# Kernel optimization log

Hardware: AMD Instinct MI355X
Metric: run time of the kernel (lower is better)

Reference implementation:

```python
import jax, jax.numpy as jnp
import numpy as np

EPS = 1e-06

def _hermite_coeffs(coord_diff, sigmas):
    # coord_diff: [B,N,K,2], sigmas: [K] -> coeff: [B,N,K,6]
    dx = coord_diff[..., 0]  # [B,N,K]
    dy = coord_diff[..., 1]
    s2 = sigmas ** 2 + EPS   # [K], broadcasts over B,N
    s4 = sigmas ** 4 + EPS
    ones = jnp.ones_like(dx)
    # idx order follows nested (order, alpha) loop of the torch code:
    # (0,0), (0,1)->-dy, (1,0)->-dx, (0,2), (1,1), (2,0)
    coeff = jnp.stack([
        ones,
        -dy / s2,
        -dx / s2,
        dy ** 2 / s4 - 1.0 / s2,
        dx * dy / s4,
        dx ** 2 / s4 - 1.0 / s2,
    ], axis=-1)  # [B,N,K,6]
    return coeff


def setup_inputs() -> dict:
    key = jax.random.key(0)
    k1, k2, k3, k4, k5 = jax.random.split(key, 5)
    B, N, K, H, O = 4, 65536, 32, 6, 31
    return {
        "mlp_output": jax.random.normal(k1, (B, N, O), dtype=jnp.float32),
        "coord_diff": jax.random.normal(k2, (B, N, K, 2), dtype=jnp.float32),
        "sigmas": jax.random.uniform(k3, (K,), dtype=jnp.float32, minval=0.1, maxval=1.0),
        "gaussian_weights": jax.random.uniform(k4, (B, N, K), dtype=jnp.float32),
        "rbf_weights": jax.random.normal(k5, (K, H, O), dtype=jnp.float32),
    }


def reference(mlp_output, coord_diff, sigmas, gaussian_weights, rbf_weights):
    # final[b,n,o] = mlp_output[b,n,o] * sum_{k,h} coeff[b,n,k,h]*gw[b,n,k]*W[k,h,o]
    coeff = _hermite_coeffs(coord_diff, sigmas)            # [B,N,K,6]
    mix = jnp.einsum('bnkh,bnk,kho->bno', coeff, gaussian_weights, rbf_weights)
    return mlp_output * mix
```

## Files before the change

### kernel.cpp

```cpp
#include <hip/hip_runtime.h>

#define KK 32
#define HH 6
#define OO 31
#define KT 16
#define EPS 1e-6f

__global__ __launch_bounds__(256, 4) void hermite_fused_kernel(
    const float* __restrict__ mlp,
    const float* __restrict__ cd,
    const float* __restrict__ sigmas,
    const float* __restrict__ gw,
    const float* __restrict__ W,
    float* __restrict__ out,
    int P)
{
    __shared__ float s_i2[KK];
    __shared__ float s_i4[KK];

    const int tid = threadIdx.x;
    if (tid < KK) {
        float s = sigmas[tid];
        s_i2[tid] = 1.0f / (s * s + EPS);
        s_i4[tid] = 1.0f / (s * s * s * s + EPS);
    }
    __syncthreads();

    const int p = blockIdx.x * blockDim.x + tid;
    if (p >= P) return;

    const float4* __restrict__ cdv = (const float4*)(cd + (size_t)p * (KK * 2));
    const float4* __restrict__ gwv = (const float4*)(gw + (size_t)p * KK);

    float acc[OO];
#pragma unroll
    for (int o = 0; o < OO; ++o) acc[o] = 0.0f;

#pragma unroll 1
    for (int kt = 0; kt < KK / KT; ++kt) {
        float cf[KT * 2];
        float gf[KT];
#pragma unroll
        for (int i = 0; i < KT / 2; ++i) {
            float4 t = cdv[kt * (KT / 2) + i];
            cf[4 * i + 0] = t.x;
            cf[4 * i + 1] = t.y;
            cf[4 * i + 2] = t.z;
            cf[4 * i + 3] = t.w;
        }
#pragma unroll
        for (int i = 0; i < KT / 4; ++i) {
            float4 t = gwv[kt * (KT / 4) + i];
            gf[4 * i + 0] = t.x;
            gf[4 * i + 1] = t.y;
            gf[4 * i + 2] = t.z;
            gf[4 * i + 3] = t.w;
        }

#pragma unroll
        for (int j = 0; j < KT; ++j) {
            const int k = kt * KT + j;
            float dx = cf[2 * j + 0];
            float dy = cf[2 * j + 1];
            float g  = gf[j];
            float i2 = s_i2[k];
            float i4 = s_i4[k];

            float t2 = g * i2;
            float t4 = g * i4;
            float dxt4 = dx * t4;
            float dyt4 = dy * t4;

            float d0 = g;
            float d1 = -dy * t2;
            float d2 = -dx * t2;
            float d3 = fmaf(dy, dyt4, -t2);
            float d4 = dx * dyt4;
            float d5 = fmaf(dx, dxt4, -t2);

            const float* __restrict__ Wk = W + k * (HH * OO);
#pragma unroll
            for (int o = 0; o < OO; ++o) {
                float a = acc[o];
                a = fmaf(d0, Wk[0 * OO + o], a);
                a = fmaf(d1, Wk[1 * OO + o], a);
                a = fmaf(d2, Wk[2 * OO + o], a);
                a = fmaf(d3, Wk[3 * OO + o], a);
                a = fmaf(d4, Wk[4 * OO + o], a);
                a = fmaf(d5, Wk[5 * OO + o], a);
                acc[o] = a;
            }
        }
    }

    const size_t base = (size_t)p * OO;
#pragma unroll
    for (int o = 0; o < OO; ++o) {
        out[base + o] = mlp[base + o] * acc[o];
    }
}

extern "C" void kernel_launch(void* const* d_in, const int* in_sizes, int n_in,
                              void* d_out, int out_size, void* d_ws, size_t ws_size,
                              hipStream_t stream) {
    const float* mlp    = (const float*)d_in[0];
    const float* cd     = (const float*)d_in[1];
    const float* sigmas = (const float*)d_in[2];
    const float* gw     = (const float*)d_in[3];
    const float* W      = (const float*)d_in[4];
    float* out          = (float*)d_out;

    const int P = in_sizes[3] / KK;
    const int block = 256;
    const int grid = (P + block - 1) / block;

    hermite_fused_kernel<<<grid, block, 0, stream>>>(mlp, cd, sigmas, gw, W, out, P);
}
```

Before: 215.6 us.

## Stage W in LDS and coalesce the output epilogue via shared-memory transpose

The weight tensor W (32x6x31 floats) is copied into shared memory at block start, so the inner FMA loop reads it from LDS rather than through scalar or global loads. The per-thread accumulators are then written to shared memory and read back as float4, so the mlp loads and output stores become coalesced vector accesses instead of strided 31-float rows per thread. This adds a ~31KB LDS allocation per block, which may limit occupancy under the 4-blocks-per-SM launch bound, and adds extra barriers. The tail guard drops any partial float4, which is only safe when the total size is a multiple of 4.

```diff
diff --git a/kernel.cpp b/kernel.cpp
--- a/kernel.cpp
+++ b/kernel.cpp
@@ -5,6 +5,9 @@
 #define OO 31
 #define KT 16
 #define EPS 1e-6f
+
+#define KHO (KK * HH * OO)
+#define MIX_DW (256 * OO)
 
 __global__ __launch_bounds__(256, 4) void hermite_fused_kernel(
     const float* __restrict__ mlp,
@@ -15,6 +18,7 @@
     float* __restrict__ out,
     int P)
 {
+    __shared__ float smem[MIX_DW];
     __shared__ float s_i2[KK];
     __shared__ float s_i4[KK];
 
@@ -24,79 +28,110 @@
         s_i2[tid] = 1.0f / (s * s + EPS);
         s_i4[tid] = 1.0f / (s * s * s * s + EPS);
     }
+
+    {
+        const float4* __restrict__ Wv = (const float4*)W;
+        float4* sWv = (float4*)smem;
+        for (int j = tid; j < KHO / 4; j += 256) {
+            sWv[j] = Wv[j];
+        }
+    }
     __syncthreads();
 
     const int p = blockIdx.x * blockDim.x + tid;
-    if (p >= P) return;
-
-    const float4* __restrict__ cdv = (const float4*)(cd + (size_t)p * (KK * 2));
-    const float4* __restrict__ gwv = (const float4*)(gw + (size_t)p * KK);
 
     float acc[OO];
 #pragma unroll
     for (int o = 0; o < OO; ++o) acc[o] = 0.0f;
 
+    if (p < P) {
+        const float4* __restrict__ cdv = (const float4*)(cd + (size_t)p * (KK * 2));
+        const float4* __restrict__ gwv = (const float4*)(gw + (size_t)p * KK);
+
 #pragma unroll 1
-    for (int kt = 0; kt < KK / KT; ++kt) {
-        float cf[KT * 2];
-        float gf[KT];
+        for (int kt = 0; kt < KK / KT; ++kt) {
+            float cf[KT * 2];
+            float gf[KT];
 #pragma unroll
-        for (int i = 0; i < KT / 2; ++i) {
-            float4 t = cdv[kt * (KT / 2) + i];
-            cf[4 * i + 0] = t.x;
-            cf[4 * i + 1] = t.y;
-            cf[4 * i + 2] = t.z;
-            cf[4 * i + 3] = t.w;
-        }
+            for (int i = 0; i < KT / 2; ++i) {
+                float4 t = cdv[kt * (KT / 2) + i];
+                cf[4 * i + 0] = t.x;
+                cf[4 * i + 1] = t.y;
+                cf[4 * i + 2] = t.z;
+                cf[4 * i + 3] = t.w;
+            }
 #pragma unroll
-        for (int i = 0; i < KT / 4; ++i) {
-            float4 t = gwv[kt * (KT / 4) + i];
-            gf[4 * i + 0] = t.x;
-            gf[4 * i + 1] = t.y;
-            gf[4 * i + 2] = t.z;
-            gf[4 * i + 3] = t.w;
-        }
+            for (int i = 0; i < KT / 4; ++i) {
+                float4 t = gwv[kt * (KT / 4) + i];
+                gf[4 * i + 0] = t.x;
+                gf[4 * i + 1] = t.y;
+                gf[4 * i + 2] = t.z;
+                gf[4 * i + 3] = t.w;
+            }
 
 #pragma unroll
-        for (int j = 0; j < KT; ++j) {
-            const int k = kt * KT + j;
-            float dx = cf[2 * j + 0];
-            float dy = cf[2 * j + 1];
-            float g  = gf[j];
-            float i2 = s_i2[k];
-            float i4 = s_i4[k];
+            for (int j = 0; j < KT; ++j) {
+                const int k = kt * KT + j;
+                float dx = cf[2 * j + 0];
+                float dy = cf[2 * j + 1];
+                float g  = gf[j];
+                float i2 = s_i2[k];
+                float i4 = s_i4[k];
 
-            float t2 = g * i2;
-            float t4 = g * i4;
-            float dxt4 = dx * t4;
-            float dyt4 = dy * t4;
+                float t2 = g * i2;
+                float t4 = g * i4;
+                float dxt4 = dx * t4;
+                float dyt4 = dy * t4;
 
-            float d0 = g;
-            float d1 = -dy * t2;
-            float d2 = -dx * t2;
-            float d3 = fmaf(dy, dyt4, -t2);
-            float d4 = dx * dyt4;
-            float d5 = fmaf(dx, dxt4, -t2);
+                float d0 = g;
+                float d1 = -dy * t2;
+                float d2 = -dx * t2;
+                float d3 = fmaf(dy, dyt4, -t2);
+                float d4 = dx * dyt4;
+                float d5 = fmaf(dx, dxt4, -t2);
 
-            const float* __restrict__ Wk = W + k * (HH * OO);
+                const float* Wk = &smem[k * (HH * OO)];
 #pragma unroll
-            for (int o = 0; o < OO; ++o) {
-                float a = acc[o];
-                a = fmaf(d0, Wk[0 * OO + o], a);
-                a = fmaf(d1, Wk[1 * OO + o], a);
-                a = fmaf(d2, Wk[2 * OO + o], a);
-                a = fmaf(d3, Wk[3 * OO + o], a);
-                a = fmaf(d4, Wk[4 * OO + o], a);
-                a = fmaf(d5, Wk[5 * OO + o], a);
-                acc[o] = a;
+                for (int o = 0; o < OO; ++o) {
+                    float a = acc[o];
+                    a = fmaf(d0, Wk[0 * OO + o], a);
+                    a = fmaf(d1, Wk[1 * OO + o], a);
+                    a = fmaf(d2, Wk[2 * OO + o], a);
+                    a = fmaf(d3, Wk[3 * OO + o], a);
+                    a = fmaf(d4, Wk[4 * OO + o], a);
+                    a = fmaf(d5, Wk[5 * OO + o], a);
+                    acc[o] = a;
+                }
             }
         }
     }
 
-    const size_t base = (size_t)p * OO;
+    __syncthreads();
 #pragma unroll
     for (int o = 0; o < OO; ++o) {
-        out[base + o] = mlp[base + o] * acc[o];
+        smem[tid * OO + o] = acc[o];
+    }
+    __syncthreads();
+
+    {
+        const size_t blk_dw = (size_t)blockIdx.x * MIX_DW;
+        const float4* __restrict__ mlpv = (const float4*)(mlp + blk_dw);
+        float4* __restrict__ outv = (float4*)(out + blk_dw);
+        const float4* mixv = (const float4*)smem;
+        const int nf4 = MIX_DW / 4;
+        const size_t total_dw = (size_t)P * OO;
+        for (int j = tid; j < nf4; j += 256) {
+            if (blk_dw + 4 * j + 3 < total_dw) {
+                float4 m = mlpv[j];
+                float4 x = mixv[j];
+                float4 r;
+                r.x = m.x * x.x;
+                r.y = m.y * x.y;
+                r.z = m.z * x.z;
+                r.w = m.w * x.w;
+                outv[j] = r;
+            }
+        }
     }
 }
 
```

Result: no change. 217.3 us (+0.8%).
